# Kernel tuning notes

Measured on AMD Instinct MI355X. Metric: run time of the kernel, lower is better.

The kernel has to match this reference:

```python
import jax, jax.numpy as jnp
import numpy as np

R = 3            # num_relations
H = 256          # hid_dim
N0, N1, N2, N3 = 50000, 10000, 4000, 1024   # sampled node counts per hop
FAN = 16         # in-edges per target node
NB_NODES = 100000


def setup_inputs() -> dict:
    keys = iter(jax.random.split(jax.random.key(0), 80))
    def nrm(shape, scale=1.0):
        return jax.random.normal(next(keys), shape, jnp.float32) * scale
    inp = {}
    inp["features"] = nrm((NB_NODES, H))
    inp["n_ids"] = jax.random.randint(next(keys), (R, N0), 0, NB_NODES)
    def edges(n_src, n_dst):
        src = jax.random.randint(next(keys), (R, n_dst * FAN), 0, n_src)
        dst = jnp.tile(jnp.repeat(jnp.arange(n_dst), FAN)[None, :], (R, 1))
        return src, dst
    inp["src1"], inp["dst1"] = edges(N0, N1)
    inp["src2"], inp["dst2"] = edges(N1, N2)
    inp["src3"], inp["dst3"] = edges(N2, N3)
    def tconv_params(p, din, heads, ch):
        hc = heads * ch
        s = 1.0 / np.sqrt(din)
        for nm in ("Wq", "Wk", "Wv", "Ws"):
            inp[p + nm] = nrm((R, din, hc), s)
        for nm in ("bq", "bk", "bv", "bs"):
            inp[p + nm] = jnp.zeros((R, hc), jnp.float32)
        inp[p + "Wb"] = nrm((R, 3 * hc, 1), 1.0 / np.sqrt(3 * hc))
    tconv_params("l1_", H, 2, H // 2)
    tconv_params("l2_", H, 1, H // 2)
    tconv_params("l3_", H // 2, 1, H)
    inp["w_omega"] = nrm((H, H), 1.0 / np.sqrt(H))
    inp["b_omega"] = jnp.zeros((H,), jnp.float32)
    inp["u_omega"] = nrm((H,), 1.0 / np.sqrt(H))
    inp["rl"] = jnp.ones((R, 1), jnp.float32)
    return inp


def _tconv(x, src, dst, n_dst, P, heads, ch):
    """PyG TransformerConv with beta=True (gated skip), concat heads, eval mode."""
    Wq, bq, Wk, bk, Wv, bv, Ws, bs, Wb = P
    x_dst = x[:n_dst]
    q = (x_dst @ Wq + bq).reshape(n_dst, heads, ch)
    k = (x @ Wk + bk).reshape(-1, heads, ch)
    v = (x @ Wv + bv).reshape(-1, heads, ch)
    logit = (q[dst] * k[src]).sum(-1) * (1.0 / np.sqrt(ch))        # [E, heads]
    m = jax.ops.segment_max(logit, dst, num_segments=n_dst)
    p = jnp.exp(logit - m[dst])
    z = jax.ops.segment_sum(p, dst, num_segments=n_dst)
    a = p / z[dst]                                                  # edge softmax
    out = jax.ops.segment_sum(v[src] * a[..., None], dst, num_segments=n_dst)
    out = out.reshape(n_dst, heads * ch)
    x_r = x_dst @ Ws + bs
    g = jax.nn.sigmoid(jnp.concatenate([out, x_r, out - x_r], -1) @ Wb)
    return g * x_r + (1.0 - g) * out


def _rel_forward(feats, n_id, s1, d1, s2, d2, s3, d3, P1, P2, P3):
    x = feats[n_id]                                     # [N0, H]
    x = _tconv(x, s1, d1, N1, P1, 2, H // 2)            # [N1, H]
    x = (x - x.mean(0)) / jnp.sqrt(x.var(0) + 1e-5)     # BatchNorm1d (batch stats, identity affine)
    x = jax.nn.elu(x)
    x = _tconv(x, s2, d2, N2, P2, 1, H // 2)            # [N2, H/2]
    x = _tconv(x, s3, d3, N3, P3, 1, H)                 # [N3, H]
    return x


def _forward(features, n_ids, src1, dst1, src2, dst2, src3, dst3,
             l1_Wq, l1_bq, l1_Wk, l1_bk, l1_Wv, l1_bv, l1_Ws, l1_bs, l1_Wb,
             l2_Wq, l2_bq, l2_Wk, l2_bk, l2_Wv, l2_bv, l2_Ws, l2_bs, l2_Wb,
             l3_Wq, l3_bq, l3_Wk, l3_bk, l3_Wv, l3_bv, l3_Ws, l3_bs, l3_Wb,
             w_omega, b_omega, u_omega, rl):
    P1 = (l1_Wq, l1_bq, l1_Wk, l1_bk, l1_Wv, l1_bv, l1_Ws, l1_bs, l1_Wb)
    P2 = (l2_Wq, l2_bq, l2_Wk, l2_bk, l2_Wv, l2_bv, l2_Ws, l2_bs, l2_Wb)
    P3 = (l3_Wq, l3_bq, l3_Wk, l3_bk, l3_Wv, l3_bv, l3_Ws, l3_bs, l3_Wb)
    per_rel = jax.vmap(_rel_forward, in_axes=(None, 0, 0, 0, 0, 0, 0, 0, 0, 0, 0))
    emb = per_rel(features, n_ids, src1, dst1, src2, dst2, src3, dst3, P1, P2, P3)  # [R, N3, H]
    multi = emb.transpose(1, 0, 2) * rl[None]            # [N3, R, H], RL-threshold scaled
    v = jnp.tanh(multi @ w_omega + b_omega)              # [N3, R, H]
    alphas = jax.nn.softmax(v @ u_omega, axis=1)         # [N3, R]
    return (multi * alphas[..., None]).sum(1)            # [N3, H]


def reference(features, n_ids, src1, dst1, src2, dst2, src3, dst3,
              l1_Wq, l1_bq, l1_Wk, l1_bk, l1_Wv, l1_bv, l1_Ws, l1_bs, l1_Wb,
              l2_Wq, l2_bq, l2_Wk, l2_bk, l2_Wv, l2_bv, l2_Ws, l2_bs, l2_Wb,
              l3_Wq, l3_bq, l3_Wk, l3_bk, l3_Wv, l3_bv, l3_Ws, l3_bs, l3_Wb,
              w_omega, b_omega, u_omega, rl):
    return _forward(features, n_ids, src1, dst1, src2, dst2, src3, dst3,
                    l1_Wq, l1_bq, l1_Wk, l1_bk, l1_Wv, l1_bv, l1_Ws, l1_bs, l1_Wb,
                    l2_Wq, l2_bq, l2_Wk, l2_bk, l2_Wv, l2_bv, l2_Ws, l2_bs, l2_Wb,
                    l3_Wq, l3_bq, l3_Wk, l3_bk, l3_Wv, l3_bv, l3_Ws, l3_bs, l3_Wb,
                    w_omega, b_omega, u_omega, rl)
```

## Files before the change

### kernel.cpp

```cpp
#include <hip/hip_runtime.h>
#include <hip/hip_bf16.h>
#include <math.h>

#define H 256
#define N0 50000
#define N1 10000
#define N2 4000
#define N3 1024
#define FAN 16

typedef __hip_bfloat16 bf16;
typedef __attribute__((ext_vector_type(8))) short short8;
typedef __attribute__((ext_vector_type(4))) short short4v;
typedef __attribute__((ext_vector_type(2))) short short2v;
typedef __attribute__((ext_vector_type(4))) float floatx4;

typedef const __attribute__((address_space(1))) void* gas_ptr;
typedef __attribute__((address_space(3))) void* las_ptr;

__device__ __forceinline__ void load_lds16(const void* g, void* l) {
    __builtin_amdgcn_global_load_lds((gas_ptr)g, (las_ptr)l, 16, 0, 0);
}

__device__ __forceinline__ float2 cvt_bf2(unsigned u) {
    union { unsigned q; float f; } lo, hi;
    lo.q = u << 16; hi.q = u & 0xffff0000u;
    return make_float2(lo.f, hi.f);
}

template<int K>
__global__ __launch_bounds__(256, 4) void gemm_dual(
    const bf16* __restrict__ A, size_t Astr,
    const bf16* __restrict__ BtKV, const bf16* __restrict__ BtQS,
    const float* __restrict__ bk, const float* __restrict__ bv,
    const float* __restrict__ bq, const float* __restrict__ bs, int Nh,
    bf16* __restrict__ Ckv, size_t CkvStr, int Mkv,
    float* __restrict__ Cqs, size_t CqsStr, int Mqs,
    int nbKV)
{
    constexpr int KC = K / 32;
    constexpr int CPR = K / 8;
    constexpr int LOG_CPR = (K == 256) ? 5 : 4;
    constexpr int RPI = 64 / CPR;
    constexpr int ISSUES = 16 / RPI;
    const int N = 2 * Nh;
    __shared__ bf16 A_s[64 * K];

    const int z = blockIdx.z;
    const bool isKV = (int)blockIdx.x < nbKV;
    const int bx = isKV ? blockIdx.x : blockIdx.x - nbKV;
    const int M = isKV ? Mkv : Mqs;
    const bf16* Bt = (isKV ? BtKV : BtQS) + (size_t)z * N * K;
    const float* b1 = (isKV ? bk : bq) + (size_t)z * Nh;
    const float* b2 = (isKV ? bv : bs) + (size_t)z * Nh;
    A += (size_t)z * Astr;

    const int lane = threadIdx.x & 63;
    const int w = threadIdx.x >> 6;
    const int lm = lane & 15;
    const int q = lane >> 4;
    const int mbase = bx * 64;
    const int n0 = blockIdx.y * 256;

    {
        const int ch = lane & (CPR - 1);
        const int rsub = lane >> LOG_CPR;
        #pragma unroll
        for (int i = 0; i < ISSUES; i++) {
            int row = w * 16 + i * RPI + rsub;
            int grow = mbase + row; grow = grow < M ? grow : M - 1;
            int gch = ch ^ (row & 7);
            load_lds16(A + (size_t)grow * K + gch * 8,
                       A_s + (size_t)(w * 16 + i * RPI) * K);
        }
    }

    const bf16* bp[4];
    #pragma unroll
    for (int ni = 0; ni < 4; ni++)
        bp[ni] = Bt + (size_t)(n0 + w * 64 + ni * 16 + lm) * K + q * 8;

    floatx4 acc[4][4];
    #pragma unroll
    for (int i = 0; i < 4; i++)
        #pragma unroll
        for (int j = 0; j < 4; j++)
            acc[i][j] = (floatx4){0.f, 0.f, 0.f, 0.f};

    short8 br0[4], br1[4], br2[4];
    #pragma unroll
    for (int ni = 0; ni < 4; ni++) br0[ni] = *(const short8*)(bp[ni]);
    #pragma unroll
    for (int ni = 0; ni < 4; ni++) br1[ni] = *(const short8*)(bp[ni] + 32);
    #pragma unroll
    for (int ni = 0; ni < 4; ni++) br2[ni] = *(const short8*)(bp[ni] + 64);

    __syncthreads();

    #pragma unroll
    for (int kc = 0; kc < KC; kc++) {
        short8 bc[4];
        #pragma unroll
        for (int ni = 0; ni < 4; ni++) {
            bc[ni] = br0[ni]; br0[ni] = br1[ni]; br1[ni] = br2[ni];
        }
        if (kc + 3 < KC) {
            #pragma unroll
            for (int ni = 0; ni < 4; ni++)
                br2[ni] = *(const short8*)(bp[ni] + (kc + 3) * 32);
        }
        short8 af[4];
        #pragma unroll
        for (int mi = 0; mi < 4; mi++) {
            int row = mi * 16 + lm;
            af[mi] = *(const short8*)(A_s + row * K + (((kc * 4 + q) ^ (lm & 7)) * 8));
        }
        #pragma unroll
        for (int mi = 0; mi < 4; mi++)
            #pragma unroll
            for (int ni = 0; ni < 4; ni++)
                acc[mi][ni] = __builtin_amdgcn_mfma_f32_16x16x32_bf16(
                    af[mi], bc[ni], acc[mi][ni], 0, 0, 0);
    }

    if (isKV) {
        bf16* C = Ckv + (size_t)z * CkvStr;
        __syncthreads();
        bf16* stg = A_s + (size_t)w * (16 * 72);
        #pragma unroll
        for (int p = 0; p < 4; p++) {
            #pragma unroll
            for (int ni = 0; ni < 4; ni++) {
                int colg = n0 + w * 64 + ni * 16 + lm;
                float bias = (colg < Nh) ? b1[colg] : b2[colg - Nh];
                #pragma unroll
                for (int rg = 0; rg < 4; rg++)
                    stg[(q * 4 + rg) * 72 + ni * 16 + lm] = (bf16)(acc[p][ni][rg] + bias);
            }
            #pragma unroll
            for (int it = 0; it < 2; it++) {
                int rl = it * 8 + (lane >> 3);
                int grow = mbase + p * 16 + rl;
                short8 vv = *(const short8*)(stg + rl * 72 + (lane & 7) * 8);
                if (grow < M)
                    *(short8*)(C + (size_t)grow * N + n0 + w * 64 + (lane & 7) * 8) = vv;
            }
        }
    } else {
        float* C = Cqs + (size_t)z * CqsStr;
        #pragma unroll
        for (int ni = 0; ni < 4; ni++) {
            int colg = n0 + w * 64 + ni * 16 + lm;
            float bias = (colg < Nh) ? b1[colg] : b2[colg - Nh];
            #pragma unroll
            for (int mi = 0; mi < 4; mi++) {
                int rb = mbase + mi * 16 + q * 4;
                #pragma unroll
                for (int rg = 0; rg < 4; rg++) {
                    int rr = rb + rg;
                    if (rr < M) C[(size_t)rr * N + colg] = acc[mi][ni][rg] + bias;
                }
            }
        }
    }
}

__global__ __launch_bounds__(256) void gather_bf16(
    const float* __restrict__ F, const int* __restrict__ n_ids, bf16* __restrict__ out,
    int nrows)
{
    int z = blockIdx.y;
    const int* idx = n_ids + (size_t)z * nrows;
    bf16* o = out + (size_t)z * nrows * H;
    int t = blockIdx.x * 256 + threadIdx.x;
    int row = t >> 6;
    if (row >= nrows) return;
    int c4 = (t & 63) * 4;
    float4 v = *(const float4*)(F + (size_t)idx[row] * H + c4);
    bf16 tmp[4] = {(bf16)v.x, (bf16)v.y, (bf16)v.z, (bf16)v.w};
    *(short4v*)(o + (size_t)row * H + c4) = *(const short4v*)tmp;
}

__global__ __launch_bounds__(256) void pack_all(
    const float* __restrict__ l1_Wk, const float* __restrict__ l1_Wv,
    const float* __restrict__ l1_Wq, const float* __restrict__ l1_Ws,
    const float* __restrict__ l2_Wk, const float* __restrict__ l2_Wv,
    const float* __restrict__ l2_Wq, const float* __restrict__ l2_Ws,
    const float* __restrict__ l3_Wk, const float* __restrict__ l3_Wv,
    const float* __restrict__ l3_Wq, const float* __restrict__ l3_Ws,
    bf16* __restrict__ Wkv1, bf16* __restrict__ Wqs1,
    bf16* __restrict__ Wkv2, bf16* __restrict__ Wqs2,
    bf16* __restrict__ Wkv3, bf16* __restrict__ Wqs3)
{
    int job = blockIdx.z, r = blockIdx.y, nn = blockIdx.x, k = threadIdx.x;
    const float *W1, *W2; bf16* Wt; int K, Nh;
    switch (job) {
        case 0: W1 = l1_Wk; W2 = l1_Wv; Wt = Wkv1; K = 256; Nh = 256; break;
        case 1: W1 = l1_Wq; W2 = l1_Ws; Wt = Wqs1; K = 256; Nh = 256; break;
        case 2: W1 = l2_Wk; W2 = l2_Wv; Wt = Wkv2; K = 256; Nh = 128; break;
        case 3: W1 = l2_Wq; W2 = l2_Ws; Wt = Wqs2; K = 256; Nh = 128; break;
        case 4: W1 = l3_Wk; W2 = l3_Wv; Wt = Wkv3; K = 128; Nh = 256; break;
        default: W1 = l3_Wq; W2 = l3_Ws; Wt = Wqs3; K = 128; Nh = 256; break;
    }
    if (nn >= 2 * Nh || k >= K) return;
    size_t wstride = (size_t)K * Nh;
    float v = (nn < Nh) ? W1[(size_t)r * wstride + (size_t)k * Nh + nn]
                        : W2[(size_t)r * wstride + (size_t)k * Nh + (nn - Nh)];
    Wt[(size_t)r * 2 * wstride + (size_t)nn * K + k] = (bf16)v;
}

template<int CPL, int HEADS>
__global__ __launch_bounds__(256) void attn_gate(
    const float* __restrict__ qs, size_t qsStr,
    const bf16* __restrict__ kv, size_t kvStr,
    const int* __restrict__ src,
    const float* __restrict__ Wb,
    float* __restrict__ yf, size_t yfStr,
    bf16* __restrict__ yb, size_t ybStr,
    int ndst, float scale)
{
    constexpr int hc = CPL * 64;
    constexpr int LPH = 64 / HEADS;
    const int z = blockIdx.y;
    int lane = threadIdx.x & 63;
    int d = blockIdx.x * 4 + (threadIdx.x >> 6);
    if (d >= ndst) return;
    qs += (size_t)z * qsStr;
    kv += (size_t)z * kvStr;
    src += (size_t)z * ndst * FAN;
    Wb += (size_t)z * 3 * hc;

    const float* qp = qs + (size_t)d * (2 * hc) + lane * CPL;
    float qv[CPL], xv[CPL];
    if constexpr (CPL == 2) {
        float2 a = *(const float2*)qp;
        float2 b = *(const float2*)(qp + hc);
        qv[0] = a.x; qv[1] = a.y; xv[0] = b.x; xv[1] = b.y;
    } else {
        float4 a = *(const float4*)qp;
        float4 b = *(const float4*)(qp + hc);
        qv[0] = a.x; qv[1] = a.y; qv[2] = a.z; qv[3] = a.w;
        xv[0] = b.x; xv[1] = b.y; xv[2] = b.z; xv[3] = b.w;
    }
    const int* sp = src + (size_t)d * FAN;
    int sidx[FAN];
    #pragma unroll
    for (int e = 0; e < FAN; e++) sidx[e] = sp[e];

    float part[FAN];
    #pragma unroll
    for (int e = 0; e < FAN; e++) {
        const bf16* kp = kv + (size_t)sidx[e] * (2 * hc) + lane * CPL;
        if constexpr (CPL == 2) {
            float2 kf = cvt_bf2(*(const unsigned*)kp);
            part[e] = qv[0] * kf.x + qv[1] * kf.y;
        } else {
            uint2 u = *(const uint2*)kp;
            float2 k0 = cvt_bf2(u.x), k1 = cvt_bf2(u.y);
            part[e] = qv[0] * k0.x + qv[1] * k0.y + qv[2] * k1.x + qv[3] * k1.y;
        }
    }
    float logit[FAN], mx = -1e30f;
    #pragma unroll
    for (int e = 0; e < FAN; e++) {
        float dt = part[e];
        #pragma unroll
        for (int off = LPH / 2; off > 0; off >>= 1) dt += __shfl_xor(dt, off, 64);
        dt *= scale;
        logit[e] = dt;
        mx = fmaxf(mx, dt);
    }
    float zsum = 0.f, p[FAN];
    #pragma unroll
    for (int e = 0; e < FAN; e++) { p[e] = __expf(logit[e] - mx); zsum += p[e]; }
    float inv = 1.f / zsum;

    float ov[CPL];
    #pragma unroll
    for (int j = 0; j < CPL; j++) ov[j] = 0.f;
    #pragma unroll
    for (int e = 0; e < FAN; e++) {
        const bf16* vp = kv + (size_t)sidx[e] * (2 * hc) + hc + lane * CPL;
        if constexpr (CPL == 2) {
            float2 vf = cvt_bf2(*(const unsigned*)vp);
            ov[0] += p[e] * vf.x; ov[1] += p[e] * vf.y;
        } else {
            uint2 u = *(const uint2*)vp;
            float2 v0 = cvt_bf2(u.x), v1 = cvt_bf2(u.y);
            ov[0] += p[e] * v0.x; ov[1] += p[e] * v0.y;
            ov[2] += p[e] * v1.x; ov[3] += p[e] * v1.y;
        }
    }
    #pragma unroll
    for (int j = 0; j < CPL; j++) ov[j] *= inv;

    float s = 0.f;
    #pragma unroll
    for (int j = 0; j < CPL; j++) {
        int c = lane * CPL + j;
        s += ov[j] * Wb[c] + xv[j] * Wb[hc + c] + (ov[j] - xv[j]) * Wb[2 * hc + c];
    }
    #pragma unroll
    for (int off = 32; off > 0; off >>= 1) s += __shfl_xor(s, off, 64);
    float g = 1.f / (1.f + __expf(-s));

    float yv[CPL];
    #pragma unroll
    for (int j = 0; j < CPL; j++) yv[j] = g * xv[j] + (1.f - g) * ov[j];

    if (yf) {
        float* op = yf + (size_t)z * yfStr + (size_t)d * hc + lane * CPL;
        if constexpr (CPL == 2) *(float2*)op = make_float2(yv[0], yv[1]);
        else *(float4*)op = make_float4(yv[0], yv[1], yv[2], yv[3]);
    }
    if (yb) {
        bf16* op = yb + (size_t)z * ybStr + (size_t)d * hc + lane * CPL;
        bf16 tmp[CPL];
        #pragma unroll
        for (int j = 0; j < CPL; j++) tmp[j] = (bf16)yv[j];
        if constexpr (CPL == 2) *(short2v*)op = *(const short2v*)tmp;
        else *(short4v*)op = *(const short4v*)tmp;
    }
}

__global__ __launch_bounds__(256) void colstat_partial(
    const bf16* __restrict__ x, size_t xStr, int M,
    float* __restrict__ ps, float* __restrict__ pss)
{
    int z = blockIdx.y;
    const bf16* xp = x + (size_t)z * xStr;
    int f = threadIdx.x;
    int b = blockIdx.x;
    float s = 0.f, ss = 0.f;
    for (int r = b; r < M; r += 64) {
        float v = (float)xp[(size_t)r * H + f];
        s += v; ss += v * v;
    }
    ps[((size_t)z * 64 + b) * H + f] = s;
    pss[((size_t)z * 64 + b) * H + f] = ss;
}

__global__ __launch_bounds__(256) void colfinal_norm_elu(
    const float* __restrict__ ps, const float* __restrict__ pss,
    bf16* __restrict__ x, size_t xStr, int M)
{
    int z = blockIdx.y;
    bf16* xp = x + (size_t)z * xStr;
    int c = threadIdx.x;
    float s = 0.f, ss = 0.f;
    #pragma unroll 8
    for (int b = 0; b < 64; b++) {
        s += ps[((size_t)z * 64 + b) * H + c];
        ss += pss[((size_t)z * 64 + b) * H + c];
    }
    float mu = s / M;
    float istd = rsqrtf(ss / M - mu * mu + 1e-5f);
    for (int r = blockIdx.x; r < M; r += gridDim.x) {
        float t = ((float)xp[(size_t)r * H + c] - mu) * istd;
        xp[(size_t)r * H + c] = (bf16)(t > 0.f ? t : __expf(t) - 1.0f);
    }
}

__global__ __launch_bounds__(256) void semantic_kernel(
    const float* __restrict__ emb,
    const float* __restrict__ Wo, const float* __restrict__ bo,
    const float* __restrict__ uo, const float* __restrict__ rl,
    float* __restrict__ outp)
{
    __shared__ float m_s[3][H];
    __shared__ float red[H];
    __shared__ float score_s[3];
    int n = blockIdx.x, c = threadIdx.x;
    for (int r = 0; r < 3; r++)
        m_s[r][c] = emb[((size_t)r * N3 + n) * H + c] * rl[r];
    __syncthreads();
    for (int r = 0; r < 3; r++) {
        float t = bo[c];
        for (int k2 = 0; k2 < H; k2++) t += m_s[r][k2] * Wo[k2 * H + c];
        red[c] = tanhf(t) * uo[c];
        __syncthreads();
        for (int s = 128; s > 0; s >>= 1) {
            if (c < s) red[c] += red[c + s];
            __syncthreads();
        }
        if (c == 0) score_s[r] = red[0];
        __syncthreads();
    }
    float s0 = score_s[0], s1 = score_s[1], s2 = score_s[2];
    float mx = fmaxf(s0, fmaxf(s1, s2));
    float e0 = __expf(s0 - mx), e1 = __expf(s1 - mx), e2 = __expf(s2 - mx);
    float zi = 1.0f / (e0 + e1 + e2);
    outp[(size_t)n * H + c] = (m_s[0][c] * e0 + m_s[1][c] * e1 + m_s[2][c] * e2) * zi;
}

extern "C" void kernel_launch(void* const* d_in, const int* in_sizes, int n_in,
                              void* d_out, int out_size, void* d_ws, size_t ws_size,
                              hipStream_t stream) {
    const float* features = (const float*)d_in[0];
    const int*   n_ids    = (const int*)d_in[1];
    const int*   src1     = (const int*)d_in[2];
    const int*   src2     = (const int*)d_in[4];
    const int*   src3     = (const int*)d_in[6];
    const float* l1_Wq = (const float*)d_in[8];
    const float* l1_Wk = (const float*)d_in[9];
    const float* l1_Wv = (const float*)d_in[10];
    const float* l1_Ws = (const float*)d_in[11];
    const float* l1_bq = (const float*)d_in[12];
    const float* l1_bk = (const float*)d_in[13];
    const float* l1_bv = (const float*)d_in[14];
    const float* l1_bs = (const float*)d_in[15];
    const float* l1_Wb = (const float*)d_in[16];
    const float* l2_Wq = (const float*)d_in[17];
    const float* l2_Wk = (const float*)d_in[18];
    const float* l2_Wv = (const float*)d_in[19];
    const float* l2_Ws = (const float*)d_in[20];
    const float* l2_bq = (const float*)d_in[21];
    const float* l2_bk = (const float*)d_in[22];
    const float* l2_bv = (const float*)d_in[23];
    const float* l2_bs = (const float*)d_in[24];
    const float* l2_Wb = (const float*)d_in[25];
    const float* l3_Wq = (const float*)d_in[26];
    const float* l3_Wk = (const float*)d_in[27];
    const float* l3_Wv = (const float*)d_in[28];
    const float* l3_Ws = (const float*)d_in[29];
    const float* l3_bq = (const float*)d_in[30];
    const float* l3_bk = (const float*)d_in[31];
    const float* l3_bv = (const float*)d_in[32];
    const float* l3_bs = (const float*)d_in[33];
    const float* l3_Wb = (const float*)d_in[34];
    const float* w_omega = (const float*)d_in[35];
    const float* b_omega = (const float*)d_in[36];
    const float* u_omega = (const float*)d_in[37];
    const float* rl      = (const float*)d_in[38];

    float* ws = (float*)d_ws;
    size_t o = 0;
    float* emb = ws + o; o += (size_t)3 * N3 * H;
    float* qs1 = ws + o; o += (size_t)3 * N1 * 512;
    float* qs2 = ws + o; o += (size_t)3 * N2 * 256;
    float* qs3 = ws + o; o += (size_t)3 * N3 * 512;
    float* ps  = ws + o; o += (size_t)3 * 64 * H;
    float* pss = ws + o; o += (size_t)3 * 64 * H;

    bf16* bws = (bf16*)(ws + o);
    size_t b = 0;
    bf16* Xg  = bws + b; b += (size_t)3 * N0 * H;
    bf16* kv1 = bws + b; b += (size_t)3 * N0 * 512;
    bf16* x1b = bws + b; b += (size_t)3 * N1 * 256;
    bf16* kv2 = bws + b; b += (size_t)3 * N1 * 256;
    bf16* x2b = bws + b; b += (size_t)3 * N2 * 128;
    bf16* kv3 = bws + b; b += (size_t)3 * N2 * 512;
    bf16* Wkv1 = bws + b; b += (size_t)3 * 512 * H;
    bf16* Wqs1 = bws + b; b += (size_t)3 * 512 * H;
    bf16* Wkv2 = bws + b; b += (size_t)3 * 256 * H;
    bf16* Wqs2 = bws + b; b += (size_t)3 * 256 * H;
    bf16* Wkv3 = bws + b; b += (size_t)3 * 512 * 128;
    bf16* Wqs3 = bws + b; b += (size_t)3 * 512 * 128;

    const float sc128 = 0.088388347648318447f;
    const float sc256 = 0.0625f;

    pack_all<<<dim3(512, 3, 6), 256, 0, stream>>>(
        l1_Wk, l1_Wv, l1_Wq, l1_Ws, l2_Wk, l2_Wv, l2_Wq, l2_Ws,
        l3_Wk, l3_Wv, l3_Wq, l3_Ws, Wkv1, Wqs1, Wkv2, Wqs2, Wkv3, Wqs3);

    gather_bf16<<<dim3((N0 * 64 + 255) / 256, 3), 256, 0, stream>>>(
        features, n_ids, Xg, N0);

    {
        int nbKV = (N0 + 63) / 64, nbQS = (N1 + 63) / 64;
        gemm_dual<256><<<dim3(nbKV + nbQS, 2, 3), 256, 0, stream>>>(
            Xg, (size_t)N0 * H, Wkv1, Wqs1, l1_bk, l1_bv, l1_bq, l1_bs, 256,
            kv1, (size_t)N0 * 512, N0, qs1, (size_t)N1 * 512, N1, nbKV);
    }
    attn_gate<4, 2><<<dim3((N1 + 3) / 4, 3), 256, 0, stream>>>(
        qs1, (size_t)N1 * 512, kv1, (size_t)N0 * 512, src1, l1_Wb,
        (float*)nullptr, 0, x1b, (size_t)N1 * 256, N1, sc128);
    colstat_partial<<<dim3(64, 3), 256, 0, stream>>>(x1b, (size_t)N1 * 256, N1, ps, pss);
    colfinal_norm_elu<<<dim3(128, 3), 256, 0, stream>>>(ps, pss, x1b, (size_t)N1 * 256, N1);

    {
        int nbKV = (N1 + 63) / 64, nbQS = (N2 + 63) / 64;
        gemm_dual<256><<<dim3(nbKV + nbQS, 1, 3), 256, 0, stream>>>(
            x1b, (size_t)N1 * 256, Wkv2, Wqs2, l2_bk, l2_bv, l2_bq, l2_bs, 128,
            kv2, (size_t)N1 * 256, N1, qs2, (size_t)N2 * 256, N2, nbKV);
    }
    attn_gate<2, 1><<<dim3((N2 + 3) / 4, 3), 256, 0, stream>>>(
        qs2, (size_t)N2 * 256, kv2, (size_t)N1 * 256, src2, l2_Wb,
        (float*)nullptr, 0, x2b, (size_t)N2 * 128, N2, sc128);

    {
        int nbKV = (N2 + 63) / 64, nbQS = (N3 + 63) / 64;
        gemm_dual<128><<<dim3(nbKV + nbQS, 2, 3), 256, 0, stream>>>(
            x2b, (size_t)N2 * 128, Wkv3, Wqs3, l3_bk, l3_bv, l3_bq, l3_bs, 256,
            kv3, (size_t)N2 * 512, N2, qs3, (size_t)N3 * 512, N3, nbKV);
    }
    attn_gate<4, 1><<<dim3((N3 + 3) / 4, 3), 256, 0, stream>>>(
        qs3, (size_t)N3 * 512, kv3, (size_t)N2 * 512, src3, l3_Wb,
        emb, (size_t)N3 * H, (bf16*)nullptr, 0, N3, sc256);

    semantic_kernel<<<N3, 256, 0, stream>>>(emb, w_omega, b_omega, u_omega, rl, (float*)d_out);
}
```

Baseline: 613.7 us.

## Fuse feature gather and bf16 conversion into layer-1 GEMM A-tile load

Removes the separate gather_bf16 kernel and its bf16 staging buffer. The layer-1 GEMM now reads the indexed fp32 feature rows directly, converts them to bf16, and writes them into swizzled LDS. The grid is remapped so the two N-halves of each row block sit next to each other in blockIdx.x, which should let the second half hit cache on the same gathered rows. The cost is that each row is gathered twice (once per N half), and the load is synchronous through registers instead of an async global-to-LDS load.

```diff
diff --git a/kernel.cpp b/kernel.cpp
--- a/kernel.cpp
+++ b/kernel.cpp
@@ -28,9 +28,10 @@
     return make_float2(lo.f, hi.f);
 }
 
-template<int K>
+template<int K, bool GATHER>
 __global__ __launch_bounds__(256, 4) void gemm_dual(
     const bf16* __restrict__ A, size_t Astr,
+    const float* __restrict__ F, const int* __restrict__ n_ids,
     const bf16* __restrict__ BtKV, const bf16* __restrict__ BtQS,
     const float* __restrict__ bk, const float* __restrict__ bv,
     const float* __restrict__ bq, const float* __restrict__ bs, int Nh,
@@ -47,22 +48,38 @@
     __shared__ bf16 A_s[64 * K];
 
     const int z = blockIdx.z;
-    const bool isKV = (int)blockIdx.x < nbKV;
-    const int bx = isKV ? blockIdx.x : blockIdx.x - nbKV;
+    int bxl, yhalf;
+    if constexpr (GATHER) { bxl = blockIdx.x >> 1; yhalf = blockIdx.x & 1; }
+    else                  { bxl = blockIdx.x;      yhalf = blockIdx.y; }
+    const bool isKV = bxl < nbKV;
+    const int bx = isKV ? bxl : bxl - nbKV;
     const int M = isKV ? Mkv : Mqs;
     const bf16* Bt = (isKV ? BtKV : BtQS) + (size_t)z * N * K;
     const float* b1 = (isKV ? bk : bq) + (size_t)z * Nh;
     const float* b2 = (isKV ? bv : bs) + (size_t)z * Nh;
-    A += (size_t)z * Astr;
+    if constexpr (!GATHER) A += (size_t)z * Astr;
 
     const int lane = threadIdx.x & 63;
     const int w = threadIdx.x >> 6;
     const int lm = lane & 15;
     const int q = lane >> 4;
     const int mbase = bx * 64;
-    const int n0 = blockIdx.y * 256;
-
-    {
+    const int n0 = yhalf * 256;
+
+    if constexpr (GATHER) {
+        const int* idz = n_ids + (size_t)z * N0;
+        #pragma unroll 4
+        for (int j = 0; j < 16; j++) {
+            int row = w * 16 + j;
+            int grow = mbase + row; grow = grow < M ? grow : M - 1;
+            int gidx = idz[grow];
+            float4 v = *(const float4*)(F + (size_t)gidx * H + lane * 4);
+            bf16 t4[4] = {(bf16)v.x, (bf16)v.y, (bf16)v.z, (bf16)v.w};
+            int c16 = (lane >> 1) ^ (row & 7);
+            *(short4v*)(A_s + (size_t)row * K + c16 * 8 + (lane & 1) * 4) =
+                *(const short4v*)t4;
+        }
+    } else {
         const int ch = lane & (CPR - 1);
         const int rsub = lane >> LOG_CPR;
         #pragma unroll
@@ -163,22 +180,6 @@
             }
         }
     }
-}
-
-__global__ __launch_bounds__(256) void gather_bf16(
-    const float* __restrict__ F, const int* __restrict__ n_ids, bf16* __restrict__ out,
-    int nrows)
-{
-    int z = blockIdx.y;
-    const int* idx = n_ids + (size_t)z * nrows;
-    bf16* o = out + (size_t)z * nrows * H;
-    int t = blockIdx.x * 256 + threadIdx.x;
-    int row = t >> 6;
-    if (row >= nrows) return;
-    int c4 = (t & 63) * 4;
-    float4 v = *(const float4*)(F + (size_t)idx[row] * H + c4);
-    bf16 tmp[4] = {(bf16)v.x, (bf16)v.y, (bf16)v.z, (bf16)v.w};
-    *(short4v*)(o + (size_t)row * H + c4) = *(const short4v*)tmp;
 }
 
 __global__ __launch_bounds__(256) void pack_all(
@@ -444,7 +445,6 @@
 
     bf16* bws = (bf16*)(ws + o);
     size_t b = 0;
-    bf16* Xg  = bws + b; b += (size_t)3 * N0 * H;
     bf16* kv1 = bws + b; b += (size_t)3 * N0 * 512;
     bf16* x1b = bws + b; b += (size_t)3 * N1 * 256;
     bf16* kv2 = bws + b; b += (size_t)3 * N1 * 256;
@@ -464,13 +464,12 @@
         l1_Wk, l1_Wv, l1_Wq, l1_Ws, l2_Wk, l2_Wv, l2_Wq, l2_Ws,
         l3_Wk, l3_Wv, l3_Wq, l3_Ws, Wkv1, Wqs1, Wkv2, Wqs2, Wkv3, Wqs3);
 
-    gather_bf16<<<dim3((N0 * 64 + 255) / 256, 3), 256, 0, stream>>>(
-        features, n_ids, Xg, N0);
-
     {
         int nbKV = (N0 + 63) / 64, nbQS = (N1 + 63) / 64;
-        gemm_dual<256><<<dim3(nbKV + nbQS, 2, 3), 256, 0, stream>>>(
-            Xg, (size_t)N0 * H, Wkv1, Wqs1, l1_bk, l1_bv, l1_bq, l1_bs, 256,
+        int nbTot = nbKV + nbQS;
+        gemm_dual<256, true><<<dim3(nbTot * 2, 1, 3), 256, 0, stream>>>(
+            (const bf16*)nullptr, 0, features, n_ids,
+            Wkv1, Wqs1, l1_bk, l1_bv, l1_bq, l1_bs, 256,
             kv1, (size_t)N0 * 512, N0, qs1, (size_t)N1 * 512, N1, nbKV);
     }
     attn_gate<4, 2><<<dim3((N1 + 3) / 4, 3), 256, 0, stream>>>(
@@ -481,8 +480,9 @@
 
     {
         int nbKV = (N1 + 63) / 64, nbQS = (N2 + 63) / 64;
-        gemm_dual<256><<<dim3(nbKV + nbQS, 1, 3), 256, 0, stream>>>(
-            x1b, (size_t)N1 * 256, Wkv2, Wqs2, l2_bk, l2_bv, l2_bq, l2_bs, 128,
+        gemm_dual<256, false><<<dim3(nbKV + nbQS, 1, 3), 256, 0, stream>>>(
+            x1b, (size_t)N1 * 256, (const float*)nullptr, (const int*)nullptr,
+            Wkv2, Wqs2, l2_bk, l2_bv, l2_bq, l2_bs, 128,
             kv2, (size_t)N1 * 256, N1, qs2, (size_t)N2 * 256, N2, nbKV);
     }
     attn_gate<2, 1><<<dim3((N2 + 3) / 4, 3), 256, 0, stream>>>(
@@ -491,8 +491,9 @@
 
     {
         int nbKV = (N2 + 63) / 64, nbQS = (N3 + 63) / 64;
-        gemm_dual<128><<<dim3(nbKV + nbQS, 2, 3), 256, 0, stream>>>(
-            x2b, (size_t)N2 * 128, Wkv3, Wqs3, l3_bk, l3_bv, l3_bq, l3_bs, 256,
+        gemm_dual<128, false><<<dim3(nbKV + nbQS, 2, 3), 256, 0, stream>>>(
+            x2b, (size_t)N2 * 128, (const float*)nullptr, (const int*)nullptr,
+            Wkv3, Wqs3, l3_bk, l3_bv, l3_bq, l3_bs, 256,
             kv3, (size_t)N2 * 512, N2, qs3, (size_t)N3 * 512, N3, nbKV);
     }
     attn_gate<4, 1><<<dim3((N3 + 3) / 4, 3), 256, 0, stream>>>(
```

New measurement: 617.8 us. Within noise of the previous version (+0.7%).

## Fuse feature gather into layer-1 GEMM with full-width 512-thread blocks

Applied to the files above, without the earlier changes.

Removes the separate gather_bf16 kernel and the bf16 Xg intermediate, and the layer-1 GEMM now gathers feature rows by n_ids straight into swizzled LDS as bf16. The block covers all 512 output columns with 8 waves, so the A tile is loaded once instead of once per column half. B fragments are prefetched from global memory three k-chunks ahead in registers. The KV output is staged through LDS for 16-byte bf16 stores. This cuts a full write and read of the gathered matrix, but the gather latency is no longer overlapped with other blocks' MFMA work in a separate pass, and register pressure rises.

```diff
diff --git a/kernel.cpp b/kernel.cpp
--- a/kernel.cpp
+++ b/kernel.cpp
@@ -26,6 +26,137 @@
     union { unsigned q; float f; } lo, hi;
     lo.q = u << 16; hi.q = u & 0xffff0000u;
     return make_float2(lo.f, hi.f);
+}
+
+__global__ __launch_bounds__(512, 4) void gemm_l1_fused(
+    const float* __restrict__ F, const int* __restrict__ n_ids,
+    const bf16* __restrict__ BtKV, const bf16* __restrict__ BtQS,
+    const float* __restrict__ bk, const float* __restrict__ bv,
+    const float* __restrict__ bq, const float* __restrict__ bs,
+    bf16* __restrict__ Ckv, size_t CkvStr,
+    float* __restrict__ Cqs, size_t CqsStr,
+    int nbKV)
+{
+    constexpr int K = 256, Nh = 256, N = 512, KC = K / 32;
+    __shared__ bf16 A_s[64 * K];
+
+    const int z = blockIdx.z;
+    const bool isKV = (int)blockIdx.x < nbKV;
+    const int bx = isKV ? blockIdx.x : blockIdx.x - nbKV;
+    const int M = isKV ? N0 : N1;
+    const bf16* Bt = (isKV ? BtKV : BtQS) + (size_t)z * N * K;
+    const float* b1 = (isKV ? bk : bq) + (size_t)z * Nh;
+    const float* b2 = (isKV ? bv : bs) + (size_t)z * Nh;
+
+    const int lane = threadIdx.x & 63;
+    const int w = threadIdx.x >> 6;
+    const int lm = lane & 15;
+    const int q = lane >> 4;
+    const int mbase = bx * 64;
+
+    {
+        const int* idz = n_ids + (size_t)z * N0;
+        #pragma unroll 4
+        for (int j = 0; j < 8; j++) {
+            int row = w * 8 + j;
+            int grow = mbase + row; grow = grow < M ? grow : M - 1;
+            int gidx = idz[grow];
+            float4 v = *(const float4*)(F + (size_t)gidx * H + lane * 4);
+            bf16 t4[4] = {(bf16)v.x, (bf16)v.y, (bf16)v.z, (bf16)v.w};
+            int c16 = (lane >> 1) ^ (row & 7);
+            *(short4v*)(A_s + (size_t)row * K + c16 * 8 + (lane & 1) * 4) =
+                *(const short4v*)t4;
+        }
+    }
+
+    const bf16* bp[4];
+    #pragma unroll
+    for (int ni = 0; ni < 4; ni++)
+        bp[ni] = Bt + (size_t)(w * 64 + ni * 16 + lm) * K + q * 8;
+
+    floatx4 acc[4][4];
+    #pragma unroll
+    for (int i = 0; i < 4; i++)
+        #pragma unroll
+        for (int j = 0; j < 4; j++)
+            acc[i][j] = (floatx4){0.f, 0.f, 0.f, 0.f};
+
+    short8 br0[4], br1[4], br2[4];
+    #pragma unroll
+    for (int ni = 0; ni < 4; ni++) br0[ni] = *(const short8*)(bp[ni]);
+    #pragma unroll
+    for (int ni = 0; ni < 4; ni++) br1[ni] = *(const short8*)(bp[ni] + 32);
+    #pragma unroll
+    for (int ni = 0; ni < 4; ni++) br2[ni] = *(const short8*)(bp[ni] + 64);
+
+    __syncthreads();
+
+    #pragma unroll
+    for (int kc = 0; kc < KC; kc++) {
+        short8 bc[4];
+        #pragma unroll
+        for (int ni = 0; ni < 4; ni++) {
+            bc[ni] = br0[ni]; br0[ni] = br1[ni]; br1[ni] = br2[ni];
+        }
+        if (kc + 3 < KC) {
+            #pragma unroll
+            for (int ni = 0; ni < 4; ni++)
+                br2[ni] = *(const short8*)(bp[ni] + (kc + 3) * 32);
+        }
+        short8 af[4];
+        #pragma unroll
+        for (int mi = 0; mi < 4; mi++) {
+            int row = mi * 16 + lm;
+            af[mi] = *(const short8*)(A_s + row * K + (((kc * 4 + q) ^ (lm & 7)) * 8));
+        }
+        #pragma unroll
+        for (int mi = 0; mi < 4; mi++)
+            #pragma unroll
+            for (int ni = 0; ni < 4; ni++)
+                acc[mi][ni] = __builtin_amdgcn_mfma_f32_16x16x32_bf16(
+                    af[mi], bc[ni], acc[mi][ni], 0, 0, 0);
+    }
+
+    if (isKV) {
+        bf16* C = Ckv + (size_t)z * CkvStr;
+        __syncthreads();
+        bf16* stg = A_s + (size_t)w * (16 * 72);
+        #pragma unroll
+        for (int p = 0; p < 4; p++) {
+            #pragma unroll
+            for (int ni = 0; ni < 4; ni++) {
+                int colg = w * 64 + ni * 16 + lm;
+                float bias = (colg < Nh) ? b1[colg] : b2[colg - Nh];
+                #pragma unroll
+                for (int rg = 0; rg < 4; rg++)
+                    stg[(q * 4 + rg) * 72 + ni * 16 + lm] = (bf16)(acc[p][ni][rg] + bias);
+            }
+            #pragma unroll
+            for (int it = 0; it < 2; it++) {
+                int rl = it * 8 + (lane >> 3);
+                int grow = mbase + p * 16 + rl;
+                short8 vv = *(const short8*)(stg + rl * 72 + (lane & 7) * 8);
+                if (grow < M)
+                    *(short8*)(C + (size_t)grow * N + w * 64 + (lane & 7) * 8) = vv;
+            }
+        }
+    } else {
+        float* C = Cqs + (size_t)z * CqsStr;
+        #pragma unroll
+        for (int ni = 0; ni < 4; ni++) {
+            int colg = w * 64 + ni * 16 + lm;
+            float bias = (colg < Nh) ? b1[colg] : b2[colg - Nh];
+            #pragma unroll
+            for (int mi = 0; mi < 4; mi++) {
+                int rb = mbase + mi * 16 + q * 4;
+                #pragma unroll
+                for (int rg = 0; rg < 4; rg++) {
+                    int rr = rb + rg;
+                    if (rr < M) C[(size_t)rr * N + colg] = acc[mi][ni][rg] + bias;
+                }
+            }
+        }
+    }
 }
 
 template<int K>
@@ -163,22 +294,6 @@
             }
         }
     }
-}
-
-__global__ __launch_bounds__(256) void gather_bf16(
-    const float* __restrict__ F, const int* __restrict__ n_ids, bf16* __restrict__ out,
-    int nrows)
-{
-    int z = blockIdx.y;
-    const int* idx = n_ids + (size_t)z * nrows;
-    bf16* o = out + (size_t)z * nrows * H;
-    int t = blockIdx.x * 256 + threadIdx.x;
-    int row = t >> 6;
-    if (row >= nrows) return;
-    int c4 = (t & 63) * 4;
-    float4 v = *(const float4*)(F + (size_t)idx[row] * H + c4);
-    bf16 tmp[4] = {(bf16)v.x, (bf16)v.y, (bf16)v.z, (bf16)v.w};
-    *(short4v*)(o + (size_t)row * H + c4) = *(const short4v*)tmp;
 }
 
 __global__ __launch_bounds__(256) void pack_all(
@@ -444,7 +559,6 @@
 
     bf16* bws = (bf16*)(ws + o);
     size_t b = 0;
-    bf16* Xg  = bws + b; b += (size_t)3 * N0 * H;
     bf16* kv1 = bws + b; b += (size_t)3 * N0 * 512;
     bf16* x1b = bws + b; b += (size_t)3 * N1 * 256;
     bf16* kv2 = bws + b; b += (size_t)3 * N1 * 256;
@@ -464,14 +578,11 @@
         l1_Wk, l1_Wv, l1_Wq, l1_Ws, l2_Wk, l2_Wv, l2_Wq, l2_Ws,
         l3_Wk, l3_Wv, l3_Wq, l3_Ws, Wkv1, Wqs1, Wkv2, Wqs2, Wkv3, Wqs3);
 
-    gather_bf16<<<dim3((N0 * 64 + 255) / 256, 3), 256, 0, stream>>>(
-        features, n_ids, Xg, N0);
-
     {
         int nbKV = (N0 + 63) / 64, nbQS = (N1 + 63) / 64;
-        gemm_dual<256><<<dim3(nbKV + nbQS, 2, 3), 256, 0, stream>>>(
-            Xg, (size_t)N0 * H, Wkv1, Wqs1, l1_bk, l1_bv, l1_bq, l1_bs, 256,
-            kv1, (size_t)N0 * 512, N0, qs1, (size_t)N1 * 512, N1, nbKV);
+        gemm_l1_fused<<<dim3(nbKV + nbQS, 1, 3), 512, 0, stream>>>(
+            features, n_ids, Wkv1, Wqs1, l1_bk, l1_bv, l1_bq, l1_bs,
+            kv1, (size_t)N0 * 512, qs1, (size_t)N1 * 512, nbKV);
     }
     attn_gate<4, 2><<<dim3((N1 + 3) / 4, 3), 256, 0, stream>>>(
         qs1, (size_t)N1 * 512, kv1, (size_t)N0 * 512, src1, l1_Wb,
```

Result: faster. 593.8 us (-3.2%).
